# Optimization experiments

Hardware: AMD Instinct MI355X
Metric: run time of the kernel (lower is better)

## Reference

```python
import jax, jax.numpy as jnp
import numpy as np

N_NODES = 50000
N_EDGES = 800000
HIDDEN = 64


def _init_linear(key, fan_in, fan_out):
    kw, kb = jax.random.split(key)
    lim = 1.0 / np.sqrt(fan_in)
    W = jax.random.uniform(kw, (fan_in, fan_out), jnp.float32, -lim, lim)
    b = jax.random.uniform(kb, (fan_out,), jnp.float32, -lim, lim)
    return W, b


def setup_inputs() -> dict:
    key = jax.random.key(0)
    ks = jax.random.split(key, 10)
    feat = jax.random.normal(ks[0], (N_NODES, HIDDEN), jnp.float32)
    x = jax.random.normal(ks[1], (N_NODES, 3), jnp.float32)
    src = jax.random.randint(ks[2], (N_EDGES,), 0, N_NODES, jnp.int32)
    dst = jax.random.randint(ks[3], (N_EDGES,), 0, N_NODES, jnp.int32)
    # message MLP: (2H+1) -> H -> H, relu after both layers (last_activation=mid)
    W1, b1 = _init_linear(ks[4], 2 * HIDDEN + 1, HIDDEN)
    W2, b2 = _init_linear(ks[5], HIDDEN, HIDDEN)
    # soft edge gate: H -> 1
    we, be = _init_linear(ks[6], HIDDEN, 1)
    # update MLP: H -> H -> H, relu mid, no last activation
    U1, c1 = _init_linear(ks[7], HIDDEN, HIDDEN)
    U2, c2 = _init_linear(ks[8], HIDDEN, HIDDEN)
    return dict(feat=feat, x=x, src=src, dst=dst,
                W1=W1, b1=b1, W2=W2, b2=b2, we=we, be=be,
                U1=U1, c1=c1, U2=U2, c2=c2)


def reference(feat, x, src, dst, W1, b1, W2, b2, we, be, U1, c1, U2, c2):
    # per-edge squared distance between endpoint coordinates: [E, 1]
    sqd = jnp.sum((x[src] - x[dst]) ** 2, axis=-1, keepdims=True)
    # message input: [E, 2H+1]
    msg_in = jnp.concatenate([feat[src], feat[dst], sqd], axis=-1)
    # 2-layer message MLP with relu mid and last activation
    m = jax.nn.relu(jax.nn.relu(msg_in @ W1 + b1) @ W2 + b2)
    # sigmoid soft-edge gate: [E, 1]
    gate = jax.nn.sigmoid(m @ we + be)
    # scatter-sum gated messages to destination nodes: [N, H]
    m_sum = jax.ops.segment_sum(m * gate, dst, num_segments=N_NODES)
    # node update MLP on (m_sum + feat), residual add
    h = m_sum + feat
    h_new = jax.nn.relu(h @ U1 + c1) @ U2 + c2
    return h_new + feat
```

## Files before the change

kernel.cpp:

```cpp
#include <hip/hip_runtime.h>
#include <hip/hip_bf16.h>
#include <stdint.h>

#define N_NODES 50000
#define N_EDGES 800000
#define HDIM 64
#define SCAN_N (N_NODES + 1)

#define MSG_BYTES  ((size_t)N_EDGES * HDIM * 2)
#define INT_OFF    MSG_BYTES
#define DEG_OFF    (INT_OFF)
#define OFFS_OFF   (INT_OFF + 204800)
#define POS_OFF    (INT_OFF + 409600)
#define FB_OFF     (INT_OFF + 614400)
#define W1T_OFF    (FB_OFF + (size_t)N_NODES * HDIM * 2)
#define W2T_OFF    (W1T_OFF + 16384)
#define U1T_OFF    (W2T_OFF + 8192)
#define U2T_OFF    (U1T_OFF + 8192)
#define WS_NEED    (U2T_OFF + 8192)

#define CVT_BLOCKS  1563
#define PREPW_BLOCKS 80
#define HIST_BLOCKS 1024

typedef __attribute__((ext_vector_type(8))) short short8;
typedef __attribute__((ext_vector_type(4))) float floatx4;

__device__ __forceinline__ float bf2f(unsigned short u) {
    union { unsigned int i; float f; } v; v.i = ((unsigned int)u) << 16; return v.f;
}
__device__ __forceinline__ unsigned short f2bf(float f) {
    __hip_bfloat16 h = __float2bfloat16(f);
    return *reinterpret_cast<unsigned short*>(&h);
}

__device__ __forceinline__ int detect_is_bf16(const unsigned short* p) {
    int cnt = 0;
    #pragma unroll
    for (int i = 0; i < 64; ++i) {
        unsigned short b = p[i];
        int e = (b >> 7) & 0xFF;
        cnt += ((e >= 97 && e <= 157) || (b & 0x7FFF) == 0) ? 1 : 0;
    }
    return cnt >= 56;
}

__device__ __forceinline__ float getf(const void* p, unsigned int i, int isb) {
    return isb ? bf2f(((const unsigned short*)p)[i]) : ((const float*)p)[i];
}

__device__ __forceinline__ short8 get8bf(const void* p, unsigned int i, int isb) {
    if (isb) {
        return *reinterpret_cast<const short8*>((const short*)p + i);
    } else {
        const float4 f0 = *reinterpret_cast<const float4*>((const float*)p + i);
        const float4 f1 = *reinterpret_cast<const float4*>((const float*)p + i + 4);
        short8 a;
        a[0] = (short)f2bf(f0.x); a[1] = (short)f2bf(f0.y);
        a[2] = (short)f2bf(f0.z); a[3] = (short)f2bf(f0.w);
        a[4] = (short)f2bf(f1.x); a[5] = (short)f2bf(f1.y);
        a[6] = (short)f2bf(f1.z); a[7] = (short)f2bf(f1.w);
        return a;
    }
}

#define COMPILER_FENCE() asm volatile("" ::: "memory")
#define WAIT_LDS() __builtin_amdgcn_s_waitcnt(0xC07F)

__global__ __launch_bounds__(256) void prep_kernel(
    const void* __restrict__ feat, unsigned short* __restrict__ fb,
    const void* __restrict__ W1, const void* __restrict__ W2,
    const void* __restrict__ U1, const void* __restrict__ U2,
    unsigned short* __restrict__ w1t, unsigned short* __restrict__ w2t,
    unsigned short* __restrict__ u1t, unsigned short* __restrict__ u2t,
    const int* __restrict__ dst, int* __restrict__ deg)
{
    const int b = blockIdx.x;
    if (b < CVT_BLOCKS) {
        const int isb = detect_is_bf16((const unsigned short*)feat);
        int i = (b * 256 + threadIdx.x) * 8;
        if (i >= N_NODES * HDIM) return;
        if (isb) {
            *reinterpret_cast<uint4*>(fb + i) =
                *reinterpret_cast<const uint4*>((const unsigned short*)feat + i);
        } else {
            float4 f0 = *reinterpret_cast<const float4*>((const float*)feat + i);
            float4 f1 = *reinterpret_cast<const float4*>((const float*)feat + i + 4);
            ushort4 a = {f2bf(f0.x), f2bf(f0.y), f2bf(f0.z), f2bf(f0.w)};
            ushort4 c = {f2bf(f1.x), f2bf(f1.y), f2bf(f1.z), f2bf(f1.w)};
            *reinterpret_cast<ushort4*>(fb + i)     = a;
            *reinterpret_cast<ushort4*>(fb + i + 4) = c;
        }
    } else if (b < CVT_BLOCKS + PREPW_BLOCKS) {
        const int isb = detect_is_bf16((const unsigned short*)feat);
        int idx = (b - CVT_BLOCKS) * 256 + threadIdx.x;
        if (idx < 8192) {
            int n = idx >> 7, k = idx & 127;
            w1t[idx] = f2bf(getf(W1, k * 64 + n, isb));
        } else if (idx < 12288) {
            int i = idx - 8192, n = i >> 6, k = i & 63;
            w2t[i] = f2bf(getf(W2, k * 64 + n, isb));
        } else if (idx < 16384) {
            int i = idx - 12288, n = i >> 6, k = i & 63;
            u1t[i] = f2bf(getf(U1, k * 64 + n, isb));
        } else if (idx < 20480) {
            int i = idx - 16384, n = i >> 6, k = i & 63;
            u2t[i] = f2bf(getf(U2, k * 64 + n, isb));
        }
    } else {
        int e0 = (b - CVT_BLOCKS - PREPW_BLOCKS) * 256 + threadIdx.x;
        for (int e = e0; e < N_EDGES; e += HIST_BLOCKS * 256)
            atomicAdd(&deg[dst[e]], 1);
    }
}

__global__ void scan1_kernel(const int* __restrict__ deg, int* __restrict__ part) {
    __shared__ int s[1024];
    int g = blockIdx.x * 1024 + threadIdx.x;
    s[threadIdx.x] = (g < SCAN_N) ? deg[g] : 0;
    __syncthreads();
    for (int off = 512; off > 0; off >>= 1) {
        if (threadIdx.x < off) s[threadIdx.x] += s[threadIdx.x + off];
        __syncthreads();
    }
    if (threadIdx.x == 0) part[blockIdx.x] = s[0];
}

__global__ void scan2_kernel(int* __restrict__ part, int nparts) {
    if (threadIdx.x == 0) {
        int run = 0;
        for (int i = 0; i < nparts; ++i) { int t = part[i]; part[i] = run; run += t; }
    }
}

__global__ void scan3_kernel(const int* __restrict__ deg, const int* __restrict__ part,
                             int* __restrict__ offs, int* __restrict__ pos) {
    __shared__ int s[1024];
    int g = blockIdx.x * 1024 + threadIdx.x;
    int v = (g < SCAN_N) ? deg[g] : 0;
    s[threadIdx.x] = v;
    __syncthreads();
    for (int off = 1; off < 1024; off <<= 1) {
        int t = (threadIdx.x >= off) ? s[threadIdx.x - off] : 0;
        __syncthreads();
        s[threadIdx.x] += t;
        __syncthreads();
    }
    int excl = s[threadIdx.x] - v + part[blockIdx.x];
    if (g < SCAN_N) { offs[g] = excl; pos[g] = excl; }
}

template <bool CSR>
__global__ __launch_bounds__(256, 2) void edge_kernel(
    const unsigned short* __restrict__ fbf,
    const unsigned short* __restrict__ w1t, const unsigned short* __restrict__ w2t,
    const void* __restrict__ feat, const void* __restrict__ xpos,
    const int* __restrict__ src, const int* __restrict__ dst,
    const void* __restrict__ W1, const void* __restrict__ b1,
    const void* __restrict__ W2, const void* __restrict__ b2,
    const void* __restrict__ we, const void* __restrict__ be,
    float* __restrict__ msum, unsigned int msum_cap,
    unsigned short* __restrict__ msg, int* __restrict__ pos)
{
    __shared__ __align__(16) short sW1[16][64][8];
    __shared__ __align__(16) short sW2[8][64][8];
    __shared__ __align__(16) short sA2[4][16][72];

    const int isb  = detect_is_bf16((const unsigned short*)feat);
    const int tid  = threadIdx.x;
    const int wave = tid >> 6;
    const int lane = tid & 63;
    const int l15  = lane & 15;
    const int quad = lane >> 4;

    short8 bw1[4][4];
    short8 bw2[2][4];
    if (CSR) {
        for (int i = tid; i < 16 * 64; i += 256) {
            int f = i >> 6, l = i & 63;
            int n = (f & 3) * 16 + (l & 15);
            int k0 = (f >> 2) * 32 + (l >> 4) * 8;
            *reinterpret_cast<short8*>(&sW1[f][l][0]) =
                *reinterpret_cast<const short8*>(w1t + n * 128 + k0);
        }
        for (int i = tid; i < 8 * 64; i += 256) {
            int f = i >> 6, l = i & 63;
            int n = (f & 3) * 16 + (l & 15);
            int k0 = (f >> 2) * 32 + (l >> 4) * 8;
            *reinterpret_cast<short8*>(&sW2[f][l][0]) =
                *reinterpret_cast<const short8*>(w2t + n * 64 + k0);
        }
        __syncthreads();
    } else {
        #pragma unroll
        for (int c = 0; c < 4; ++c)
            #pragma unroll
            for (int nt = 0; nt < 4; ++nt) {
                short8 b;
                #pragma unroll
                for (int j = 0; j < 8; ++j)
                    b[j] = (short)f2bf(getf(W1, (c * 32 + quad * 8 + j) * 64 + nt * 16 + l15, isb));
                bw1[c][nt] = b;
            }
        #pragma unroll
        for (int c = 0; c < 2; ++c)
            #pragma unroll
            for (int nt = 0; nt < 4; ++nt) {
                short8 b;
                #pragma unroll
                for (int j = 0; j < 8; ++j)
                    b[j] = (short)f2bf(getf(W2, (c * 32 + quad * 8 + j) * 64 + nt * 16 + l15, isb));
                bw2[c][nt] = b;
            }
    }

    float b1r[4], w1lr[4], b2r[4], wer[4];
    #pragma unroll
    for (int nt = 0; nt < 4; ++nt) {
        int n = nt * 16 + l15;
        b1r[nt]  = getf(b1, n, isb);
        w1lr[nt] = getf(W1, 128 * 64 + n, isb);
        b2r[nt]  = getf(b2, n, isb);
        wer[nt]  = getf(we, n, isb);
    }
    const float ber = getf(be, 0, isb);
    const int rowb = quad * 4;

    const int ntiles = N_EDGES / 64;
    for (int t = blockIdx.x; t < ntiles; t += gridDim.x) {
        const int ebase = t * 64 + wave * 16;

        int sidx = 0, didx = 0, slotv = 0;
        float sqd = 0.f;
        if (lane < 16) {
            int e = ebase + lane;
            sidx = src[e];
            didx = dst[e];
            if (CSR) slotv = atomicAdd(&pos[didx], 1);
            float dx = getf(xpos, sidx * 3 + 0, isb) - getf(xpos, didx * 3 + 0, isb);
            float dy = getf(xpos, sidx * 3 + 1, isb) - getf(xpos, didx * 3 + 1, isb);
            float dz = getf(xpos, sidx * 3 + 2, isb) - getf(xpos, didx * 3 + 2, isb);
            sqd = dx * dx + dy * dy + dz * dz;
        }
        const int sn     = __shfl(sidx, l15);
        const int dn_row = __shfl(didx, l15);

        floatx4 acc[4];
        #pragma unroll
        for (int nt = 0; nt < 4; ++nt) acc[nt] = (floatx4){0.f, 0.f, 0.f, 0.f};
        #pragma unroll
        for (int c = 0; c < 4; ++c) {
            const int node = (c < 2) ? sn : dn_row;
            const unsigned int aoff = (unsigned int)node * 64u + (c & 1) * 32 + quad * 8;
            short8 a;
            if (CSR) a = *reinterpret_cast<const short8*>((const short*)fbf + aoff);
            else     a = get8bf(feat, aoff, isb);
            #pragma unroll
            for (int nt = 0; nt < 4; ++nt) {
                short8 b;
                if (CSR) b = *reinterpret_cast<const short8*>(&sW1[c * 4 + nt][lane][0]);
                else     b = bw1[c][nt];
                acc[nt] = __builtin_amdgcn_mfma_f32_16x16x32_bf16(a, b, acc[nt], 0, 0, 0);
            }
        }

        float sq[4];
        #pragma unroll
        for (int r = 0; r < 4; ++r) sq[r] = __shfl(sqd, rowb + r);
        #pragma unroll
        for (int nt = 0; nt < 4; ++nt)
            #pragma unroll
            for (int r = 0; r < 4; ++r) {
                float v = fmaxf(acc[nt][r] + b1r[nt] + sq[r] * w1lr[nt], 0.f);
                sA2[wave][rowb + r][nt * 16 + l15] = (short)f2bf(v);
            }
        COMPILER_FENCE();
        WAIT_LDS();

        floatx4 acc2[4];
        #pragma unroll
        for (int nt = 0; nt < 4; ++nt) acc2[nt] = (floatx4){0.f, 0.f, 0.f, 0.f};
        #pragma unroll
        for (int c = 0; c < 2; ++c) {
            short8 a = *reinterpret_cast<const short8*>(&sA2[wave][l15][c * 32 + quad * 8]);
            #pragma unroll
            for (int nt = 0; nt < 4; ++nt) {
                short8 b;
                if (CSR) b = *reinterpret_cast<const short8*>(&sW2[c * 4 + nt][lane][0]);
                else     b = bw2[c][nt];
                acc2[nt] = __builtin_amdgcn_mfma_f32_16x16x32_bf16(a, b, acc2[nt], 0, 0, 0);
            }
        }
        COMPILER_FENCE();

        float mval[4][4];
        float part[4] = {0.f, 0.f, 0.f, 0.f};
        #pragma unroll
        for (int nt = 0; nt < 4; ++nt)
            #pragma unroll
            for (int r = 0; r < 4; ++r) {
                float v = fmaxf(acc2[nt][r] + b2r[nt], 0.f);
                mval[nt][r] = v;
                part[r] += v * wer[nt];
            }
        #pragma unroll
        for (int off = 1; off < 16; off <<= 1)
            #pragma unroll
            for (int r = 0; r < 4; ++r) part[r] += __shfl_xor(part[r], off);
        float gate[4];
        #pragma unroll
        for (int r = 0; r < 4; ++r)
            gate[r] = 1.f / (1.f + __expf(-(part[r] + ber)));

        if (CSR) {
            #pragma unroll
            for (int nt = 0; nt < 4; ++nt)
                #pragma unroll
                for (int r = 0; r < 4; ++r)
                    sA2[wave][rowb + r][nt * 16 + l15] = (short)f2bf(mval[nt][r] * gate[r]);
            COMPILER_FENCE();
            WAIT_LDS();
            int slot_r = __shfl(slotv, l15);
            const short8 v0 = *reinterpret_cast<const short8*>(&sA2[wave][l15][quad * 16]);
            const short8 v1 = *reinterpret_cast<const short8*>(&sA2[wave][l15][quad * 16 + 8]);
            unsigned short* mp = msg + (size_t)slot_r * 64 + quad * 16;
            *reinterpret_cast<short8*>(mp)     = v0;
            *reinterpret_cast<short8*>(mp + 8) = v1;
            COMPILER_FENCE();
        } else {
            #pragma unroll
            for (int r = 0; r < 4; ++r) {
                int dn = __shfl(didx, rowb + r);
                unsigned int base = (unsigned int)dn * 64u;
                if (base + 64u <= msum_cap) {
                    #pragma unroll
                    for (int nt = 0; nt < 4; ++nt)
                        unsafeAtomicAdd(&msum[base + nt * 16 + l15], mval[nt][r] * gate[r]);
                }
            }
        }
    }
}

template <bool MSGRED>
__global__ __launch_bounds__(256, 2) void node_kernel(
    const unsigned short* __restrict__ msg, const int* __restrict__ offs,
    const float* __restrict__ msum,
    const unsigned short* __restrict__ u1t, const unsigned short* __restrict__ u2t,
    const void* __restrict__ feat,
    const void* __restrict__ U1, const void* __restrict__ c1v,
    const void* __restrict__ U2, const void* __restrict__ c2v,
    void* __restrict__ out)
{
    __shared__ __align__(16) short sT[4][16][72];
    __shared__ __align__(16) float sF[4][16][68];

    const int isb  = detect_is_bf16((const unsigned short*)feat);
    const int tid  = threadIdx.x;
    const int wave = tid >> 6;
    const int lane = tid & 63;
    const int l15  = lane & 15;
    const int quad = lane >> 4;

    short8 u1f[2][4], u2f[2][4];
    if (MSGRED) {
        #pragma unroll
        for (int nt = 0; nt < 4; ++nt) {
            const int n = nt * 16 + l15;
            #pragma unroll
            for (int c = 0; c < 2; ++c) {
                u1f[c][nt] = *reinterpret_cast<const short8*>(u1t + n * 64 + c * 32 + quad * 8);
                u2f[c][nt] = *reinterpret_cast<const short8*>(u2t + n * 64 + c * 32 + quad * 8);
            }
        }
    } else {
        #pragma unroll
        for (int c = 0; c < 2; ++c)
            #pragma unroll
            for (int nt = 0; nt < 4; ++nt) {
                short8 a, b;
                #pragma unroll
                for (int j = 0; j < 8; ++j) {
                    int k = c * 32 + quad * 8 + j, n = nt * 16 + l15;
                    a[j] = (short)f2bf(getf(U1, k * 64 + n, isb));
                    b[j] = (short)f2bf(getf(U2, k * 64 + n, isb));
                }
                u1f[c][nt] = a; u2f[c][nt] = b;
            }
    }
    float c1r[4], c2r[4];
    #pragma unroll
    for (int nt = 0; nt < 4; ++nt) {
        c1r[nt] = getf(c1v, nt * 16 + l15, isb);
        c2r[nt] = getf(c2v, nt * 16 + l15, isb);
    }
    const int rowb = quad * 4;

    const int ntile = (N_NODES + 15) / 16;
    const int t = blockIdx.x * 4 + wave;
    if (t < ntile) {
        const int node = t * 16 + l15;

        float acc16[16];
        #pragma unroll
        for (int i = 0; i < 16; ++i) acc16[i] = 0.f;
        if (MSGRED) {
            float accB[16];
            #pragma unroll
            for (int i = 0; i < 16; ++i) accB[i] = 0.f;
            int s = offs[node], e = offs[node + 1];
            int j = s;
            for (; j + 1 < e; j += 2) {
                const unsigned short* p0 = msg + (size_t)j * 64 + quad * 8;
                const unsigned short* p1 = msg + (size_t)(j + 1) * 64 + quad * 8;
                short8 a0 = *reinterpret_cast<const short8*>(p0);
                short8 a1 = *reinterpret_cast<const short8*>(p0 + 32);
                short8 b0 = *reinterpret_cast<const short8*>(p1);
                short8 b1 = *reinterpret_cast<const short8*>(p1 + 32);
                #pragma unroll
                for (int i = 0; i < 8; ++i) {
                    acc16[i]     += bf2f((unsigned short)a0[i]);
                    acc16[8 + i] += bf2f((unsigned short)a1[i]);
                    accB[i]      += bf2f((unsigned short)b0[i]);
                    accB[8 + i]  += bf2f((unsigned short)b1[i]);
                }
            }
            if (j < e) {
                const unsigned short* p0 = msg + (size_t)j * 64 + quad * 8;
                short8 a0 = *reinterpret_cast<const short8*>(p0);
                short8 a1 = *reinterpret_cast<const short8*>(p0 + 32);
                #pragma unroll
                for (int i = 0; i < 8; ++i) {
                    acc16[i]     += bf2f((unsigned short)a0[i]);
                    acc16[8 + i] += bf2f((unsigned short)a1[i]);
                }
            }
            #pragma unroll
            for (int i = 0; i < 16; ++i) acc16[i] += accB[i];
        } else {
            #pragma unroll
            for (int c = 0; c < 2; ++c) {
                unsigned int off = (unsigned int)node * 64u + c * 32 + quad * 8;
                float4 m0 = *reinterpret_cast<const float4*>(msum + off);
                float4 m1 = *reinterpret_cast<const float4*>(msum + off + 4);
                acc16[c * 8 + 0] = m0.x; acc16[c * 8 + 1] = m0.y;
                acc16[c * 8 + 2] = m0.z; acc16[c * 8 + 3] = m0.w;
                acc16[c * 8 + 4] = m1.x; acc16[c * 8 + 5] = m1.y;
                acc16[c * 8 + 6] = m1.z; acc16[c * 8 + 7] = m1.w;
            }
        }

        short8 ah[2];
        #pragma unroll
        for (int c = 0; c < 2; ++c) {
            unsigned int off = (unsigned int)node * 64u + c * 32 + quad * 8;
            float hv[8];
            if (isb) {
                short8 fv = *reinterpret_cast<const short8*>((const short*)feat + off);
                #pragma unroll
                for (int j = 0; j < 8; ++j) hv[j] = bf2f((unsigned short)fv[j]);
            } else {
                float4 f0 = *reinterpret_cast<const float4*>((const float*)feat + off);
                float4 f1 = *reinterpret_cast<const float4*>((const float*)feat + off + 4);
                hv[0] = f0.x; hv[1] = f0.y; hv[2] = f0.z; hv[3] = f0.w;
                hv[4] = f1.x; hv[5] = f1.y; hv[6] = f1.z; hv[7] = f1.w;
            }
            short8 a;
            #pragma unroll
            for (int j = 0; j < 8; ++j) a[j] = (short)f2bf(acc16[c * 8 + j] + hv[j]);
            ah[c] = a;
        }

        floatx4 acc[4];
        #pragma unroll
        for (int nt = 0; nt < 4; ++nt) acc[nt] = (floatx4){0.f, 0.f, 0.f, 0.f};
        #pragma unroll
        for (int c = 0; c < 2; ++c)
            #pragma unroll
            for (int nt = 0; nt < 4; ++nt)
                acc[nt] = __builtin_amdgcn_mfma_f32_16x16x32_bf16(ah[c], u1f[c][nt], acc[nt], 0, 0, 0);

        #pragma unroll
        for (int nt = 0; nt < 4; ++nt)
            #pragma unroll
            for (int r = 0; r < 4; ++r) {
                float v = fmaxf(acc[nt][r] + c1r[nt], 0.f);
                sT[wave][rowb + r][nt * 16 + l15] = (short)f2bf(v);
            }
        COMPILER_FENCE();
        WAIT_LDS();

        floatx4 acc2[4];
        #pragma unroll
        for (int nt = 0; nt < 4; ++nt) acc2[nt] = (floatx4){0.f, 0.f, 0.f, 0.f};
        #pragma unroll
        for (int c = 0; c < 2; ++c) {
            short8 a = *reinterpret_cast<const short8*>(&sT[wave][l15][c * 32 + quad * 8]);
            #pragma unroll
            for (int nt = 0; nt < 4; ++nt)
                acc2[nt] = __builtin_amdgcn_mfma_f32_16x16x32_bf16(a, u2f[c][nt], acc2[nt], 0, 0, 0);
        }
        COMPILER_FENCE();

        #pragma unroll
        for (int nt = 0; nt < 4; ++nt)
            #pragma unroll
            for (int r = 0; r < 4; ++r)
                sF[wave][rowb + r][nt * 16 + l15] = acc2[nt][r] + c2r[nt];
        COMPILER_FENCE();
        WAIT_LDS();

        const unsigned int ob = (unsigned int)node * 64u + quad * 16;
        if (isb) {
            const unsigned short* fp = (const unsigned short*)feat + ob;
            unsigned short* op = (unsigned short*)out + ob;
            #pragma unroll
            for (int k = 0; k < 2; ++k) {
                ushort4 o0, o1;
                float4 v0 = *reinterpret_cast<const float4*>(&sF[wave][l15][quad * 16 + k * 8]);
                float4 v1 = *reinterpret_cast<const float4*>(&sF[wave][l15][quad * 16 + k * 8 + 4]);
                const ushort4 f0 = *reinterpret_cast<const ushort4*>(fp + k * 8);
                const ushort4 f1 = *reinterpret_cast<const ushort4*>(fp + k * 8 + 4);
                o0.x = f2bf(v0.x + bf2f(f0.x)); o0.y = f2bf(v0.y + bf2f(f0.y));
                o0.z = f2bf(v0.z + bf2f(f0.z)); o0.w = f2bf(v0.w + bf2f(f0.w));
                o1.x = f2bf(v1.x + bf2f(f1.x)); o1.y = f2bf(v1.y + bf2f(f1.y));
                o1.z = f2bf(v1.z + bf2f(f1.z)); o1.w = f2bf(v1.w + bf2f(f1.w));
                *reinterpret_cast<ushort4*>(op + k * 8)     = o0;
                *reinterpret_cast<ushort4*>(op + k * 8 + 4) = o1;
            }
        } else {
            const float* fp = (const float*)feat + ob;
            float* op = (float*)out + ob;
            #pragma unroll
            for (int k = 0; k < 4; ++k) {
                float4 v = *reinterpret_cast<const float4*>(&sF[wave][l15][quad * 16 + k * 4]);
                float4 f = *reinterpret_cast<const float4*>(fp + k * 4);
                float4 o = {v.x + f.x, v.y + f.y, v.z + f.z, v.w + f.w};
                *reinterpret_cast<float4*>(op + k * 4) = o;
            }
        }
        COMPILER_FENCE();
    }
}

extern "C" void kernel_launch(void* const* d_in, const int* in_sizes, int n_in,
                              void* d_out, int out_size, void* d_ws, size_t ws_size,
                              hipStream_t stream) {
    const void* feat = d_in[0];
    const void* x    = d_in[1];
    const int* src   = (const int*)d_in[2];
    const int* dst   = (const int*)d_in[3];
    const void* W1   = d_in[4];
    const void* b1   = d_in[5];
    const void* W2   = d_in[6];
    const void* b2   = d_in[7];
    const void* we   = d_in[8];
    const void* be   = d_in[9];
    const void* U1   = d_in[10];
    const void* c1   = d_in[11];
    const void* U2   = d_in[12];
    const void* c2   = d_in[13];
    char* ws = (char*)d_ws;

    if (ws_size >= WS_NEED) {
        unsigned short* msg = (unsigned short*)(ws);
        int* deg  = (int*)(ws + DEG_OFF);
        int* offs = (int*)(ws + OFFS_OFF);
        int* pos  = (int*)(ws + POS_OFF);
        unsigned short* fb  = (unsigned short*)(ws + FB_OFF);
        unsigned short* w1t = (unsigned short*)(ws + W1T_OFF);
        unsigned short* w2t = (unsigned short*)(ws + W2T_OFF);
        unsigned short* u1t = (unsigned short*)(ws + U1T_OFF);
        unsigned short* u2t = (unsigned short*)(ws + U2T_OFF);

        hipMemsetAsync(deg, 0, 204800, stream);
        prep_kernel<<<CVT_BLOCKS + PREPW_BLOCKS + HIST_BLOCKS, 256, 0, stream>>>(
            feat, fb, W1, W2, U1, U2, w1t, w2t, u1t, u2t, dst, deg);
        scan1_kernel<<<49, 1024, 0, stream>>>(deg, offs + 51200 - 64);
        scan2_kernel<<<1, 64, 0, stream>>>(offs + 51200 - 64, 49);
        scan3_kernel<<<49, 1024, 0, stream>>>(deg, offs + 51200 - 64, offs, pos);
        edge_kernel<true><<<2500, 256, 0, stream>>>(fb, w1t, w2t, feat, x, src, dst,
                                                    W1, b1, W2, b2, we, be,
                                                    nullptr, 0xFFFFFFFFu, msg, pos);
        node_kernel<true><<<((N_NODES + 15) / 16 + 3) / 4, 256, 0, stream>>>(
            msg, offs, nullptr, u1t, u2t, feat, U1, c1, U2, c2, d_out);
    } else {
        float* msum = (float*)ws;
        size_t need = (size_t)N_NODES * HDIM * sizeof(float);
        size_t clr  = need < ws_size ? need : ws_size;
        unsigned int cap = (unsigned int)(ws_size / sizeof(float));
        if (cap > (unsigned int)(N_NODES * HDIM)) cap = (unsigned int)(N_NODES * HDIM);

        hipMemsetAsync(msum, 0, clr, stream);
        edge_kernel<false><<<2500, 256, 0, stream>>>(nullptr, nullptr, nullptr, feat, x, src, dst,
                                                     W1, b1, W2, b2, we, be,
                                                     msum, cap, nullptr, nullptr);
        node_kernel<false><<<((N_NODES + 15) / 16 + 3) / 4, 256, 0, stream>>>(
            nullptr, nullptr, msum, nullptr, nullptr, feat, U1, c1, U2, c2, d_out);
    }
}
```

Before: 254.2 us.

## Fuse three-pass scan into one kernel and software-prefetch edge gathers

Replaces the three scan kernels (block reduce, serial partial scan, block scan) with a single 1024-thread kernel in which each thread serially scans 49 elements before a block-level scan. This removes two launches and their dependencies. The edge kernel now prefetches the next tile's indices, slot atomics, squared distances and feature rows into registers while computing the current tile, to hide gather latency. The cost is higher register pressure under launch_bounds(256,2), and the single-block scan reads with a strided, uncoalesced per-thread pattern.

```diff
diff --git a/kernel.cpp b/kernel.cpp
--- a/kernel.cpp
+++ b/kernel.cpp
@@ -114,40 +114,39 @@
     }
 }
 
-__global__ void scan1_kernel(const int* __restrict__ deg, int* __restrict__ part) {
+__global__ __launch_bounds__(1024) void scan_fused_kernel(
+    const int* __restrict__ deg, int* __restrict__ offs, int* __restrict__ pos)
+{
     __shared__ int s[1024];
-    int g = blockIdx.x * 1024 + threadIdx.x;
-    s[threadIdx.x] = (g < SCAN_N) ? deg[g] : 0;
-    __syncthreads();
-    for (int off = 512; off > 0; off >>= 1) {
-        if (threadIdx.x < off) s[threadIdx.x] += s[threadIdx.x + off];
-        __syncthreads();
-    }
-    if (threadIdx.x == 0) part[blockIdx.x] = s[0];
-}
-
-__global__ void scan2_kernel(int* __restrict__ part, int nparts) {
-    if (threadIdx.x == 0) {
-        int run = 0;
-        for (int i = 0; i < nparts; ++i) { int t = part[i]; part[i] = run; run += t; }
-    }
-}
-
-__global__ void scan3_kernel(const int* __restrict__ deg, const int* __restrict__ part,
-                             int* __restrict__ offs, int* __restrict__ pos) {
-    __shared__ int s[1024];
-    int g = blockIdx.x * 1024 + threadIdx.x;
-    int v = (g < SCAN_N) ? deg[g] : 0;
-    s[threadIdx.x] = v;
+    const int tid = threadIdx.x;
+    const int base = tid * 49;
+    int loc[49];
+    int sum = 0;
+    #pragma unroll
+    for (int k = 0; k < 49; ++k) {
+        int g = base + k;
+        int v = (g < SCAN_N) ? deg[g] : 0;
+        loc[k] = sum;
+        sum += v;
+    }
+    s[tid] = sum;
     __syncthreads();
     for (int off = 1; off < 1024; off <<= 1) {
-        int t = (threadIdx.x >= off) ? s[threadIdx.x - off] : 0;
+        int t = (tid >= off) ? s[tid - off] : 0;
         __syncthreads();
-        s[threadIdx.x] += t;
+        s[tid] += t;
         __syncthreads();
     }
-    int excl = s[threadIdx.x] - v + part[blockIdx.x];
-    if (g < SCAN_N) { offs[g] = excl; pos[g] = excl; }
+    const int excl = s[tid] - sum;
+    #pragma unroll
+    for (int k = 0; k < 49; ++k) {
+        int g = base + k;
+        if (g < SCAN_N) {
+            int val = excl + loc[k];
+            offs[g] = val;
+            pos[g]  = val;
+        }
+    }
 }
 
 template <bool CSR>
@@ -227,46 +226,83 @@
     const int rowb = quad * 4;
 
     const int ntiles = N_EDGES / 64;
-    for (int t = blockIdx.x; t < ntiles; t += gridDim.x) {
-        const int ebase = t * 64 + wave * 16;
-
-        int sidx = 0, didx = 0, slotv = 0;
-        float sqd = 0.f;
+    const int stride = (int)gridDim.x;
+
+    int csid = 0, cdid = 0, cslot = 0;
+    float csqd = 0.f;
+    short8 ca[4];
+    #pragma unroll
+    for (int c = 0; c < 4; ++c) ca[c] = short8{0,0,0,0,0,0,0,0};
+
+    const int t0 = blockIdx.x;
+    if (t0 < ntiles) {
         if (lane < 16) {
-            int e = ebase + lane;
-            sidx = src[e];
-            didx = dst[e];
-            if (CSR) slotv = atomicAdd(&pos[didx], 1);
-            float dx = getf(xpos, sidx * 3 + 0, isb) - getf(xpos, didx * 3 + 0, isb);
-            float dy = getf(xpos, sidx * 3 + 1, isb) - getf(xpos, didx * 3 + 1, isb);
-            float dz = getf(xpos, sidx * 3 + 2, isb) - getf(xpos, didx * 3 + 2, isb);
-            sqd = dx * dx + dy * dy + dz * dz;
-        }
-        const int sn     = __shfl(sidx, l15);
-        const int dn_row = __shfl(didx, l15);
+            int e = t0 * 64 + wave * 16 + lane;
+            csid = src[e];
+            cdid = dst[e];
+            if (CSR) cslot = atomicAdd(&pos[cdid], 1);
+            float dx = getf(xpos, csid * 3 + 0, isb) - getf(xpos, cdid * 3 + 0, isb);
+            float dy = getf(xpos, csid * 3 + 1, isb) - getf(xpos, cdid * 3 + 1, isb);
+            float dz = getf(xpos, csid * 3 + 2, isb) - getf(xpos, cdid * 3 + 2, isb);
+            csqd = dx * dx + dy * dy + dz * dz;
+        }
+        const int sn = __shfl(csid, l15);
+        const int dn = __shfl(cdid, l15);
+        #pragma unroll
+        for (int c = 0; c < 4; ++c) {
+            const int node = (c < 2) ? sn : dn;
+            const unsigned int aoff = (unsigned int)node * 64u + (c & 1) * 32 + quad * 8;
+            if (CSR) ca[c] = *reinterpret_cast<const short8*>((const short*)fbf + aoff);
+            else     ca[c] = get8bf(feat, aoff, isb);
+        }
+    }
+
+    for (int t = t0; t < ntiles; t += stride) {
+        int nsid = 0, ndid = 0, nslot = 0;
+        float nsqd = 0.f;
+        short8 na[4];
+        #pragma unroll
+        for (int c = 0; c < 4; ++c) na[c] = ca[c];
+        const int tn = t + stride;
+        if (tn < ntiles) {
+            if (lane < 16) {
+                int e = tn * 64 + wave * 16 + lane;
+                nsid = src[e];
+                ndid = dst[e];
+                if (CSR) nslot = atomicAdd(&pos[ndid], 1);
+                float dx = getf(xpos, nsid * 3 + 0, isb) - getf(xpos, ndid * 3 + 0, isb);
+                float dy = getf(xpos, nsid * 3 + 1, isb) - getf(xpos, ndid * 3 + 1, isb);
+                float dz = getf(xpos, nsid * 3 + 2, isb) - getf(xpos, ndid * 3 + 2, isb);
+                nsqd = dx * dx + dy * dy + dz * dz;
+            }
+            const int sn = __shfl(nsid, l15);
+            const int dn = __shfl(ndid, l15);
+            #pragma unroll
+            for (int c = 0; c < 4; ++c) {
+                const int node = (c < 2) ? sn : dn;
+                const unsigned int aoff = (unsigned int)node * 64u + (c & 1) * 32 + quad * 8;
+                if (CSR) na[c] = *reinterpret_cast<const short8*>((const short*)fbf + aoff);
+                else     na[c] = get8bf(feat, aoff, isb);
+            }
+        }
 
         floatx4 acc[4];
         #pragma unroll
         for (int nt = 0; nt < 4; ++nt) acc[nt] = (floatx4){0.f, 0.f, 0.f, 0.f};
         #pragma unroll
         for (int c = 0; c < 4; ++c) {
-            const int node = (c < 2) ? sn : dn_row;
-            const unsigned int aoff = (unsigned int)node * 64u + (c & 1) * 32 + quad * 8;
-            short8 a;
-            if (CSR) a = *reinterpret_cast<const short8*>((const short*)fbf + aoff);
-            else     a = get8bf(feat, aoff, isb);
             #pragma unroll
             for (int nt = 0; nt < 4; ++nt) {
                 short8 b;
                 if (CSR) b = *reinterpret_cast<const short8*>(&sW1[c * 4 + nt][lane][0]);
                 else     b = bw1[c][nt];
-                acc[nt] = __builtin_amdgcn_mfma_f32_16x16x32_bf16(a, b, acc[nt], 0, 0, 0);
+                acc[nt] = __builtin_amdgcn_mfma_f32_16x16x32_bf16(ca[c], b, acc[nt], 0, 0, 0);
             }
         }
 
         float sq[4];
         #pragma unroll
-        for (int r = 0; r < 4; ++r) sq[r] = __shfl(sqd, rowb + r);
+        for (int r = 0; r < 4; ++r) sq[r] = __shfl(csqd, rowb + r);
         #pragma unroll
         for (int nt = 0; nt < 4; ++nt)
             #pragma unroll
@@ -320,7 +356,7 @@
                     sA2[wave][rowb + r][nt * 16 + l15] = (short)f2bf(mval[nt][r] * gate[r]);
             COMPILER_FENCE();
             WAIT_LDS();
-            int slot_r = __shfl(slotv, l15);
+            int slot_r = __shfl(cslot, l15);
             const short8 v0 = *reinterpret_cast<const short8*>(&sA2[wave][l15][quad * 16]);
             const short8 v1 = *reinterpret_cast<const short8*>(&sA2[wave][l15][quad * 16 + 8]);
             unsigned short* mp = msg + (size_t)slot_r * 64 + quad * 16;
@@ -330,7 +366,7 @@
         } else {
             #pragma unroll
             for (int r = 0; r < 4; ++r) {
-                int dn = __shfl(didx, rowb + r);
+                int dn = __shfl(cdid, rowb + r);
                 unsigned int base = (unsigned int)dn * 64u;
                 if (base + 64u <= msum_cap) {
                     #pragma unroll
@@ -339,6 +375,10 @@
                 }
             }
         }
+
+        csid = nsid; cdid = ndid; cslot = nslot; csqd = nsqd;
+        #pragma unroll
+        for (int c = 0; c < 4; ++c) ca[c] = na[c];
     }
 }
 
@@ -576,9 +616,7 @@
         hipMemsetAsync(deg, 0, 204800, stream);
         prep_kernel<<<CVT_BLOCKS + PREPW_BLOCKS + HIST_BLOCKS, 256, 0, stream>>>(
             feat, fb, W1, W2, U1, U2, w1t, w2t, u1t, u2t, dst, deg);
-        scan1_kernel<<<49, 1024, 0, stream>>>(deg, offs + 51200 - 64);
-        scan2_kernel<<<1, 64, 0, stream>>>(offs + 51200 - 64, 49);
-        scan3_kernel<<<49, 1024, 0, stream>>>(deg, offs + 51200 - 64, offs, pos);
+        scan_fused_kernel<<<1, 1024, 0, stream>>>(deg, offs, pos);
         edge_kernel<true><<<2500, 256, 0, stream>>>(fb, w1t, w2t, feat, x, src, dst,
                                                     W1, b1, W2, b2, we, be,
                                                     nullptr, 0xFFFFFFFFu, msg, pos);
```

Result: slower. 319.8 us (+25.8%).

## Sort edges by destination and segment-reduce messages with float atomics

Applied to the files above, without the earlier changes.

Adds a permute kernel that scatters packed (src, dst, sqd) records into destination-sorted order. The edge kernel then reads these records and run-length reduces consecutive rows with equal destination before issuing float atomics into a zeroed node-sum buffer. This replaces writing a bf16 per-edge message array and CSR-reducing it in the node kernel. It cuts the message write/read traffic but adds an extra permutation pass and atomics, and the summation order becomes nondeterministic.

```diff
diff --git a/kernel.cpp b/kernel.cpp
--- a/kernel.cpp
+++ b/kernel.cpp
@@ -7,21 +7,22 @@
 #define HDIM 64
 #define SCAN_N (N_NODES + 1)
 
-#define MSG_BYTES  ((size_t)N_EDGES * HDIM * 2)
-#define INT_OFF    MSG_BYTES
-#define DEG_OFF    (INT_OFF)
-#define OFFS_OFF   (INT_OFF + 204800)
-#define POS_OFF    (INT_OFF + 409600)
-#define FB_OFF     (INT_OFF + 614400)
+#define MSUM_OFF   0
+#define EP_OFF     12800000
+#define DEG_OFF    (EP_OFF + 12800000)
+#define OFFS_OFF   (DEG_OFF + 204800)
+#define POS_OFF    (OFFS_OFF + 204800)
+#define FB_OFF     (POS_OFF + 204800)
 #define W1T_OFF    (FB_OFF + (size_t)N_NODES * HDIM * 2)
 #define W2T_OFF    (W1T_OFF + 16384)
 #define U1T_OFF    (W2T_OFF + 8192)
 #define U2T_OFF    (U1T_OFF + 8192)
 #define WS_NEED    (U2T_OFF + 8192)
 
-#define CVT_BLOCKS  1563
+#define CVT_BLOCKS   1563
 #define PREPW_BLOCKS 80
-#define HIST_BLOCKS 1024
+#define MZ_BLOCKS    3125
+#define HIST_BLOCKS  1024
 
 typedef __attribute__((ext_vector_type(8))) short short8;
 typedef __attribute__((ext_vector_type(4))) float floatx4;
@@ -73,7 +74,8 @@
     const void* __restrict__ U1, const void* __restrict__ U2,
     unsigned short* __restrict__ w1t, unsigned short* __restrict__ w2t,
     unsigned short* __restrict__ u1t, unsigned short* __restrict__ u2t,
-    const int* __restrict__ dst, int* __restrict__ deg)
+    const int* __restrict__ dst, int* __restrict__ deg,
+    uint4* __restrict__ msumz)
 {
     const int b = blockIdx.x;
     if (b < CVT_BLOCKS) {
@@ -107,8 +109,12 @@
             int i = idx - 16384, n = i >> 6, k = i & 63;
             u2t[i] = f2bf(getf(U2, k * 64 + n, isb));
         }
+    } else if (b < CVT_BLOCKS + PREPW_BLOCKS + MZ_BLOCKS) {
+        int i = (b - CVT_BLOCKS - PREPW_BLOCKS) * 256 + threadIdx.x;
+        if (i < N_NODES * HDIM / 4)
+            msumz[i] = (uint4){0u, 0u, 0u, 0u};
     } else {
-        int e0 = (b - CVT_BLOCKS - PREPW_BLOCKS) * 256 + threadIdx.x;
+        int e0 = (b - CVT_BLOCKS - PREPW_BLOCKS - MZ_BLOCKS) * 256 + threadIdx.x;
         for (int e = e0; e < N_EDGES; e += HIST_BLOCKS * 256)
             atomicAdd(&deg[dst[e]], 1);
     }
@@ -150,21 +156,45 @@
     if (g < SCAN_N) { offs[g] = excl; pos[g] = excl; }
 }
 
+__global__ __launch_bounds__(256) void permute_kernel(
+    const void* __restrict__ feat, const void* __restrict__ xpos,
+    const int* __restrict__ src, const int* __restrict__ dst,
+    int* __restrict__ pos, uint4* __restrict__ epack)
+{
+    const int isb = detect_is_bf16((const unsigned short*)feat);
+    int e = blockIdx.x * 256 + threadIdx.x;
+    if (e < N_EDGES) {
+        int s = src[e], d = dst[e];
+        int slot = atomicAdd(&pos[d], 1);
+        float dx = getf(xpos, s * 3 + 0, isb) - getf(xpos, d * 3 + 0, isb);
+        float dy = getf(xpos, s * 3 + 1, isb) - getf(xpos, d * 3 + 1, isb);
+        float dz = getf(xpos, s * 3 + 2, isb) - getf(xpos, d * 3 + 2, isb);
+        float sqd = dx * dx + dy * dy + dz * dz;
+        uint4 p;
+        p.x = (unsigned int)s;
+        p.y = (unsigned int)d;
+        p.z = __float_as_uint(sqd);
+        p.w = 0u;
+        epack[slot] = p;
+    }
+}
+
 template <bool CSR>
 __global__ __launch_bounds__(256, 2) void edge_kernel(
     const unsigned short* __restrict__ fbf,
     const unsigned short* __restrict__ w1t, const unsigned short* __restrict__ w2t,
     const void* __restrict__ feat, const void* __restrict__ xpos,
     const int* __restrict__ src, const int* __restrict__ dst,
+    const uint4* __restrict__ epack,
     const void* __restrict__ W1, const void* __restrict__ b1,
     const void* __restrict__ W2, const void* __restrict__ b2,
     const void* __restrict__ we, const void* __restrict__ be,
-    float* __restrict__ msum, unsigned int msum_cap,
-    unsigned short* __restrict__ msg, int* __restrict__ pos)
+    float* __restrict__ msum, unsigned int msum_cap)
 {
     __shared__ __align__(16) short sW1[16][64][8];
     __shared__ __align__(16) short sW2[8][64][8];
     __shared__ __align__(16) short sA2[4][16][72];
+    __shared__ int sD[4][16];
 
     const int isb  = detect_is_bf16((const unsigned short*)feat);
     const int tid  = threadIdx.x;
@@ -230,17 +260,26 @@
     for (int t = blockIdx.x; t < ntiles; t += gridDim.x) {
         const int ebase = t * 64 + wave * 16;
 
-        int sidx = 0, didx = 0, slotv = 0;
+        int sidx = 0, didx = 0;
         float sqd = 0.f;
-        if (lane < 16) {
-            int e = ebase + lane;
-            sidx = src[e];
-            didx = dst[e];
-            if (CSR) slotv = atomicAdd(&pos[didx], 1);
-            float dx = getf(xpos, sidx * 3 + 0, isb) - getf(xpos, didx * 3 + 0, isb);
-            float dy = getf(xpos, sidx * 3 + 1, isb) - getf(xpos, didx * 3 + 1, isb);
-            float dz = getf(xpos, sidx * 3 + 2, isb) - getf(xpos, didx * 3 + 2, isb);
-            sqd = dx * dx + dy * dy + dz * dz;
+        if (CSR) {
+            if (lane < 16) {
+                uint4 p = epack[ebase + lane];
+                sidx = (int)p.x;
+                didx = (int)p.y;
+                sqd  = __uint_as_float(p.z);
+                sD[wave][lane] = didx;
+            }
+        } else {
+            if (lane < 16) {
+                int e = ebase + lane;
+                sidx = src[e];
+                didx = dst[e];
+                float dx = getf(xpos, sidx * 3 + 0, isb) - getf(xpos, didx * 3 + 0, isb);
+                float dy = getf(xpos, sidx * 3 + 1, isb) - getf(xpos, didx * 3 + 1, isb);
+                float dz = getf(xpos, sidx * 3 + 2, isb) - getf(xpos, didx * 3 + 2, isb);
+                sqd = dx * dx + dy * dy + dz * dz;
+            }
         }
         const int sn     = __shfl(sidx, l15);
         const int dn_row = __shfl(didx, l15);
@@ -320,12 +359,18 @@
                     sA2[wave][rowb + r][nt * 16 + l15] = (short)f2bf(mval[nt][r] * gate[r]);
             COMPILER_FENCE();
             WAIT_LDS();
-            int slot_r = __shfl(slotv, l15);
-            const short8 v0 = *reinterpret_cast<const short8*>(&sA2[wave][l15][quad * 16]);
-            const short8 v1 = *reinterpret_cast<const short8*>(&sA2[wave][l15][quad * 16 + 8]);
-            unsigned short* mp = msg + (size_t)slot_r * 64 + quad * 16;
-            *reinterpret_cast<short8*>(mp)     = v0;
-            *reinterpret_cast<short8*>(mp + 8) = v1;
+            float run = 0.f;
+            int dcur = sD[wave][0];
+            #pragma unroll
+            for (int r = 0; r < 16; ++r) {
+                run += bf2f((unsigned short)sA2[wave][r][lane]);
+                int dnxt = (r < 15) ? sD[wave][r + 1] : -1;
+                if (dnxt != dcur) {
+                    unsafeAtomicAdd(&msum[(unsigned int)dcur * 64u + lane], run);
+                    run = 0.f;
+                    dcur = dnxt;
+                }
+            }
             COMPILER_FENCE();
         } else {
             #pragma unroll
@@ -342,9 +387,7 @@
     }
 }
 
-template <bool MSGRED>
 __global__ __launch_bounds__(256, 2) void node_kernel(
-    const unsigned short* __restrict__ msg, const int* __restrict__ offs,
     const float* __restrict__ msum,
     const unsigned short* __restrict__ u1t, const unsigned short* __restrict__ u2t,
     const void* __restrict__ feat,
@@ -363,7 +406,7 @@
     const int quad = lane >> 4;
 
     short8 u1f[2][4], u2f[2][4];
-    if (MSGRED) {
+    if (u1t) {
         #pragma unroll
         for (int nt = 0; nt < 4; ++nt) {
             const int n = nt * 16 + l15;
@@ -401,59 +444,13 @@
     if (t < ntile) {
         const int node = t * 16 + l15;
 
-        float acc16[16];
-        #pragma unroll
-        for (int i = 0; i < 16; ++i) acc16[i] = 0.f;
-        if (MSGRED) {
-            float accB[16];
-            #pragma unroll
-            for (int i = 0; i < 16; ++i) accB[i] = 0.f;
-            int s = offs[node], e = offs[node + 1];
-            int j = s;
-            for (; j + 1 < e; j += 2) {
-                const unsigned short* p0 = msg + (size_t)j * 64 + quad * 8;
-                const unsigned short* p1 = msg + (size_t)(j + 1) * 64 + quad * 8;
-                short8 a0 = *reinterpret_cast<const short8*>(p0);
-                short8 a1 = *reinterpret_cast<const short8*>(p0 + 32);
-                short8 b0 = *reinterpret_cast<const short8*>(p1);
-                short8 b1 = *reinterpret_cast<const short8*>(p1 + 32);
-                #pragma unroll
-                for (int i = 0; i < 8; ++i) {
-                    acc16[i]     += bf2f((unsigned short)a0[i]);
-                    acc16[8 + i] += bf2f((unsigned short)a1[i]);
-                    accB[i]      += bf2f((unsigned short)b0[i]);
-                    accB[8 + i]  += bf2f((unsigned short)b1[i]);
-                }
-            }
-            if (j < e) {
-                const unsigned short* p0 = msg + (size_t)j * 64 + quad * 8;
-                short8 a0 = *reinterpret_cast<const short8*>(p0);
-                short8 a1 = *reinterpret_cast<const short8*>(p0 + 32);
-                #pragma unroll
-                for (int i = 0; i < 8; ++i) {
-                    acc16[i]     += bf2f((unsigned short)a0[i]);
-                    acc16[8 + i] += bf2f((unsigned short)a1[i]);
-                }
-            }
-            #pragma unroll
-            for (int i = 0; i < 16; ++i) acc16[i] += accB[i];
-        } else {
-            #pragma unroll
-            for (int c = 0; c < 2; ++c) {
-                unsigned int off = (unsigned int)node * 64u + c * 32 + quad * 8;
-                float4 m0 = *reinterpret_cast<const float4*>(msum + off);
-                float4 m1 = *reinterpret_cast<const float4*>(msum + off + 4);
-                acc16[c * 8 + 0] = m0.x; acc16[c * 8 + 1] = m0.y;
-                acc16[c * 8 + 2] = m0.z; acc16[c * 8 + 3] = m0.w;
-                acc16[c * 8 + 4] = m1.x; acc16[c * 8 + 5] = m1.y;
-                acc16[c * 8 + 6] = m1.z; acc16[c * 8 + 7] = m1.w;
-            }
-        }
-
         short8 ah[2];
         #pragma unroll
         for (int c = 0; c < 2; ++c) {
             unsigned int off = (unsigned int)node * 64u + c * 32 + quad * 8;
+            float4 m0 = *reinterpret_cast<const float4*>(msum + off);
+            float4 m1 = *reinterpret_cast<const float4*>(msum + off + 4);
+            float mv[8] = {m0.x, m0.y, m0.z, m0.w, m1.x, m1.y, m1.z, m1.w};
             float hv[8];
             if (isb) {
                 short8 fv = *reinterpret_cast<const short8*>((const short*)feat + off);
@@ -467,7 +464,7 @@
             }
             short8 a;
             #pragma unroll
-            for (int j = 0; j < 8; ++j) a[j] = (short)f2bf(acc16[c * 8 + j] + hv[j]);
+            for (int j = 0; j < 8; ++j) a[j] = (short)f2bf(mv[j] + hv[j]);
             ah[c] = a;
         }
 
@@ -563,7 +560,8 @@
     char* ws = (char*)d_ws;
 
     if (ws_size >= WS_NEED) {
-        unsigned short* msg = (unsigned short*)(ws);
+        float* msum = (float*)(ws + MSUM_OFF);
+        uint4* epack = (uint4*)(ws + EP_OFF);
         int* deg  = (int*)(ws + DEG_OFF);
         int* offs = (int*)(ws + OFFS_OFF);
         int* pos  = (int*)(ws + POS_OFF);
@@ -574,16 +572,17 @@
         unsigned short* u2t = (unsigned short*)(ws + U2T_OFF);
 
         hipMemsetAsync(deg, 0, 204800, stream);
-        prep_kernel<<<CVT_BLOCKS + PREPW_BLOCKS + HIST_BLOCKS, 256, 0, stream>>>(
-            feat, fb, W1, W2, U1, U2, w1t, w2t, u1t, u2t, dst, deg);
+        prep_kernel<<<CVT_BLOCKS + PREPW_BLOCKS + MZ_BLOCKS + HIST_BLOCKS, 256, 0, stream>>>(
+            feat, fb, W1, W2, U1, U2, w1t, w2t, u1t, u2t, dst, deg, (uint4*)msum);
         scan1_kernel<<<49, 1024, 0, stream>>>(deg, offs + 51200 - 64);
         scan2_kernel<<<1, 64, 0, stream>>>(offs + 51200 - 64, 49);
         scan3_kernel<<<49, 1024, 0, stream>>>(deg, offs + 51200 - 64, offs, pos);
-        edge_kernel<true><<<2500, 256, 0, stream>>>(fb, w1t, w2t, feat, x, src, dst,
+        permute_kernel<<<(N_EDGES + 255) / 256, 256, 0, stream>>>(feat, x, src, dst, pos, epack);
+        edge_kernel<true><<<2500, 256, 0, stream>>>(fb, w1t, w2t, feat, x, src, dst, epack,
                                                     W1, b1, W2, b2, we, be,
-                                                    nullptr, 0xFFFFFFFFu, msg, pos);
-        node_kernel<true><<<((N_NODES + 15) / 16 + 3) / 4, 256, 0, stream>>>(
-            msg, offs, nullptr, u1t, u2t, feat, U1, c1, U2, c2, d_out);
+                                                    msum, (unsigned int)(N_NODES * HDIM));
+        node_kernel<<<((N_NODES + 15) / 16 + 3) / 4, 256, 0, stream>>>(
+            msum, u1t, u2t, feat, U1, c1, U2, c2, d_out);
     } else {
         float* msum = (float*)ws;
         size_t need = (size_t)N_NODES * HDIM * sizeof(float);
@@ -593,9 +592,9 @@
 
         hipMemsetAsync(msum, 0, clr, stream);
         edge_kernel<false><<<2500, 256, 0, stream>>>(nullptr, nullptr, nullptr, feat, x, src, dst,
-                                                     W1, b1, W2, b2, we, be,
-                                                     msum, cap, nullptr, nullptr);
-        node_kernel<false><<<((N_NODES + 15) / 16 + 3) / 4, 256, 0, stream>>>(
-            nullptr, nullptr, msum, nullptr, nullptr, feat, U1, c1, U2, c2, d_out);
-    }
-}
+                                                     nullptr, W1, b1, W2, b2, we, be,
+                                                     msum, cap);
+        node_kernel<<<((N_NODES + 15) / 16 + 3) / 4, 256, 0, stream>>>(
+            msum, nullptr, nullptr, feat, U1, c1, U2, c2, d_out);
+    }
+}
```

Result: slower. 273.1 us (+7.4%).
